# Optimization experiments

Hardware: AMD Instinct MI355X
Metric: run time of the kernel (lower is better)

## Reference

```python
import jax, jax.numpy as jnp
from jax import lax
import numpy as np

ALPHA = 0.5
MAX_ITERS = 40
TOL = 1e-6
BITS = 8


def fake_quant_sym(w, bits=BITS):
    # symmetric per-tensor fake quantisation
    qmax = float(2 ** (bits - 1) - 1)
    scale = jnp.max(jnp.abs(w)) / qmax
    return jnp.round(w / scale) * scale


def fb_solve(Wq, Uq, bq, x, alpha=ALPHA, max_iters=MAX_ITERS, tol=TOL):
    # forward-backward splitting fixed-point solve: z = relu((1-a)z + a(Wz + Ux^T + b))
    n = Wq.shape[0]
    B = x.shape[0]
    Ux = Uq @ x.T + bq[:, None]  # (n, B), constant across iterations

    def cond(carry):
        z, res, it = carry
        return jnp.logical_and(it < max_iters, res >= tol)

    def body(carry):
        z, _, it = carry
        u = (1.0 - alpha) * z + alpha * (Wq @ z + Ux)
        z_next = jax.nn.relu(u)  # relu_prox
        res = jnp.linalg.norm(z_next - z) / (jnp.linalg.norm(z) + 1e-12)
        return z_next, res, it + 1

    z0 = jnp.zeros((n, B), dtype=x.dtype)
    z, _, _ = lax.while_loop(cond, body, (z0, jnp.array(jnp.inf, dtype=x.dtype), 0))
    u_star = (1.0 - alpha) * z + alpha * (Wq @ z + Ux)
    mask = (u_star > 0).astype(x.dtype)  # relu Jacobian mask D*
    return z, mask


def setup_inputs() -> dict:
    key = jax.random.key(0)
    k0, k1, k2, k3, k4 = jax.random.split(key, 5)
    n, d, B, C = 512, 784, 128, 10
    # scale W so ||W||_2 < 1 (monotone operator condition m > 0)
    W = 0.3 * jax.random.normal(k0, (n, n), dtype=jnp.float32) / jnp.sqrt(n)
    U = jax.random.normal(k1, (n, d), dtype=jnp.float32) / jnp.sqrt(d)
    b = 0.01 * jax.random.normal(k2, (n,), dtype=jnp.float32)
    x = jax.random.normal(k3, (B, d), dtype=jnp.float32)
    Wc = jax.random.normal(k4, (C, n), dtype=jnp.float32) / jnp.sqrt(n)
    bc = jnp.zeros((C,), dtype=jnp.float32)
    return {"W": W, "U": U, "b": b, "x": x, "Wc": Wc, "bc": bc}


def reference(W, U, b, x, Wc, bc):
    # post-training fake quantisation of W, U, b (done once at init in torch)
    Wq = fake_quant_sym(W)
    Uq = fake_quant_sym(U)
    bq = fake_quant_sym(b)
    z_star, _ = fb_solve(Wq, Uq, bq, x)  # (n, B)
    logits = z_star.T @ Wc.T + bc  # classifier on z*^T
    return logits
```

## Files before the change

kernel.cpp:

```cpp
#include <hip/hip_runtime.h>
#include <hip/hip_bf16.h>


#define N_DIM 512
#define D_DIM 784
#define B_DIM 128
#define C_DIM 10
#define QMAX 127.0f
#define N_ITERS 40
#define HILO_START 28
#define ZPITCH 528
#define MT 2
#define UPITCH 808

typedef int    i32x4  __attribute__((ext_vector_type(4)));
typedef float  f32x4  __attribute__((ext_vector_type(4)));
typedef __bf16 bf16x8 __attribute__((ext_vector_type(8)));
typedef short  s16x2  __attribute__((ext_vector_type(2)));

__device__ __forceinline__ void pack_hl(const int vq[4], unsigned int& h, unsigned int& l) {
    int pk01, pk23;
#if __has_builtin(__builtin_amdgcn_cvt_pk_i16)
    union { s16x2 v; int i; } u0, u1;
    u0.v = __builtin_amdgcn_cvt_pk_i16(vq[0], vq[1]);
    u1.v = __builtin_amdgcn_cvt_pk_i16(vq[2], vq[3]);
    pk01 = u0.i; pk23 = u1.i;
#else
    asm("v_cvt_pk_i16_i32 %0, %1, %2" : "=v"(pk01) : "v"(vq[0]), "v"(vq[1]));
    asm("v_cvt_pk_i16_i32 %0, %1, %2" : "=v"(pk23) : "v"(vq[2]), "v"(vq[3]));
#endif
    h = __builtin_amdgcn_perm((unsigned int)pk23, (unsigned int)pk01, 0x07050301u);
    l = __builtin_amdgcn_perm((unsigned int)pk23, (unsigned int)pk01, 0x06040200u) ^ 0x80808080u;
}

__global__ __launch_bounds__(256) void prep_kernel(const float* __restrict__ W,
                                                   const float* __restrict__ U,
                                                   const float* __restrict__ b,
                                                   const float* __restrict__ x,
                                                   int* __restrict__ sync,
                                                   signed char* __restrict__ Qp8,
                                                   float* __restrict__ UxT) {
    __shared__ __bf16 xhS[16][UPITCH];
    __shared__ __bf16 xlS[16][UPITCH];
    __shared__ f32x4  sacc[4][64];
    __shared__ float  smax[3];
    const int t = threadIdx.x;
    const int wave = t >> 6, lane = t & 63;

    {
        const int gid = blockIdx.x * 256 + t;
        float mW = 0.0f, mU = 0.0f, mB = 0.0f;
        if (gid < N_DIM * N_DIM / 4) {
            float4 v = ((const float4*)W)[gid];
            mW = fmaxf(fmaxf(fabsf(v.x), fabsf(v.y)), fmaxf(fabsf(v.z), fabsf(v.w)));
        }
        if (gid < N_DIM * D_DIM / 4) {
            float4 v = ((const float4*)U)[gid];
            mU = fmaxf(fmaxf(fabsf(v.x), fabsf(v.y)), fmaxf(fabsf(v.z), fabsf(v.w)));
        }
        if (gid < N_DIM / 4) {
            float4 v = ((const float4*)b)[gid];
            mB = fmaxf(fmaxf(fabsf(v.x), fabsf(v.y)), fmaxf(fabsf(v.z), fabsf(v.w)));
        }
#pragma unroll
        for (int s = 1; s < 64; s <<= 1) {
            mW = fmaxf(mW, __shfl_xor(mW, s));
            mU = fmaxf(mU, __shfl_xor(mU, s));
            mB = fmaxf(mB, __shfl_xor(mB, s));
        }
        float* ls = (float*)sacc;
        if (lane == 0) { ls[wave * 3 + 0] = mW; ls[wave * 3 + 1] = mU; ls[wave * 3 + 2] = mB; }
        __syncthreads();
        if (t == 0) {
            float aW = fmaxf(fmaxf(ls[0], ls[3]), fmaxf(ls[6], ls[9]));
            float aU = fmaxf(fmaxf(ls[1], ls[4]), fmaxf(ls[7], ls[10]));
            float aB = fmaxf(fmaxf(ls[2], ls[5]), fmaxf(ls[8], ls[11]));
            atomicMax(&sync[1], __float_as_int(aW));
            atomicMax(&sync[2], __float_as_int(aU));
            atomicMax(&sync[3], __float_as_int(aB));
            __hip_atomic_fetch_add(&sync[0], 1, __ATOMIC_ACQ_REL, __HIP_MEMORY_SCOPE_AGENT);
            while (__hip_atomic_load(&sync[0], __ATOMIC_ACQUIRE, __HIP_MEMORY_SCOPE_AGENT)
                   < (int)gridDim.x)
                __builtin_amdgcn_s_sleep(2);
            smax[0] = __int_as_float(__hip_atomic_load(&sync[1], __ATOMIC_RELAXED, __HIP_MEMORY_SCOPE_AGENT));
            smax[1] = __int_as_float(__hip_atomic_load(&sync[2], __ATOMIC_RELAXED, __HIP_MEMORY_SCOPE_AGENT));
            smax[2] = __int_as_float(__hip_atomic_load(&sync[3], __ATOMIC_RELAXED, __HIP_MEMORY_SCOPE_AGENT));
        }
        __syncthreads();
    }

    if (blockIdx.x < 256) {
        const float s = smax[0] * (1.0f / QMAX);
        const float inv = 1.0f / s;
        int idx = blockIdx.x * 256 + t;
        float4 w = ((const float4*)W)[idx];
        int k = (idx << 2) & (N_DIM - 1);
        int r = (idx << 2) >> 9;
        char4 c;
        c.x = (signed char)(int)rintf(w.x * inv);
        c.y = (signed char)(int)rintf(w.y * inv);
        c.z = (signed char)(int)rintf(w.z * inv);
        c.w = (signed char)(int)rintf(w.w * inv);
        int kc = k >> 6, q = (k >> 4) & 3, jj = k & 15;
        *(char4*)&Qp8[((kc << 9) + r) * 64 + q * 16 + jj] = c;
    } else {
        const float sU = smax[1] * (1.0f / QMAX);
        const float invU = 1.0f / sU;
        const float sb = smax[2] * (1.0f / QMAX);
        const int bx = blockIdx.x - 256;
        const int i0 = (bx >> 3) * 16;
        const int c0 = (bx & 7) * 16;
        for (int i = t; i < 16 * 196; i += 256) {
            int r = i / 196, kf = i - r * 196;
            float4 v = *(const float4*)&x[(c0 + r) * D_DIM + (kf << 2)];
            union { __bf16 e[4]; ushort4 u; } hh, ll;
            float f0 = v.x, f1 = v.y, f2 = v.z, f3 = v.w;
            __bf16 h0 = (__bf16)f0, h1 = (__bf16)f1, h2 = (__bf16)f2, h3 = (__bf16)f3;
            hh.e[0] = h0; hh.e[1] = h1; hh.e[2] = h2; hh.e[3] = h3;
            ll.e[0] = (__bf16)(f0 - (float)h0);
            ll.e[1] = (__bf16)(f1 - (float)h1);
            ll.e[2] = (__bf16)(f2 - (float)h2);
            ll.e[3] = (__bf16)(f3 - (float)h3);
            *(ushort4*)&xhS[r][kf << 2] = hh.u;
            *(ushort4*)&xlS[r][kf << 2] = ll.u;
        }
        {
            int r = t >> 4, k = D_DIM + (t & 15);
            xhS[r][k] = (__bf16)0.0f; xlS[r][k] = (__bf16)0.0f;
        }
        __syncthreads();
        const int m = lane & 15, quad = lane >> 4;
        f32x4 acc = {};
        for (int kc = wave; kc < 25; kc += 4) {
            const int k0 = (kc << 5) + (quad << 3);
            bf16x8 au = {};
            if (k0 < D_DIM) {
                const float4 u0 = *(const float4*)&U[(i0 + m) * D_DIM + k0];
                const float4 u1 = *(const float4*)&U[(i0 + m) * D_DIM + k0 + 4];
                au[0] = (__bf16)rintf(u0.x * invU); au[1] = (__bf16)rintf(u0.y * invU);
                au[2] = (__bf16)rintf(u0.z * invU); au[3] = (__bf16)rintf(u0.w * invU);
                au[4] = (__bf16)rintf(u1.x * invU); au[5] = (__bf16)rintf(u1.y * invU);
                au[6] = (__bf16)rintf(u1.z * invU); au[7] = (__bf16)rintf(u1.w * invU);
            }
            bf16x8 bh = *(const bf16x8*)&xhS[m][k0];
            bf16x8 bl = *(const bf16x8*)&xlS[m][k0];
            acc = __builtin_amdgcn_mfma_f32_16x16x32_bf16(au, bh, acc, 0, 0, 0);
            acc = __builtin_amdgcn_mfma_f32_16x16x32_bf16(au, bl, acc, 0, 0, 0);
        }
        sacc[wave][lane] = acc;
        __syncthreads();
        if (wave == 0) {
            f32x4 s0 = sacc[0][lane], s1 = sacc[1][lane];
            f32x4 s2 = sacc[2][lane], s3 = sacc[3][lane];
            const int row0 = i0 + (quad << 2);
            f32x4 o;
#pragma unroll
            for (int r = 0; r < 4; ++r)
                o[r] = sU * (s0[r] + s1[r] + s2[r] + s3[r])
                     + rintf(b[row0 + r] / sb) * sb;
            *(f32x4*)&UxT[(c0 + m) * N_DIM + row0] = o;
        }
    }
}

__global__ __launch_bounds__(1024, 1) void solve_kernel(const signed char* __restrict__ Qp8,
                                                        const float* __restrict__ UxT,
                                                        const float* __restrict__ wsf,
                                                        const float* __restrict__ Wc,
                                                        const float* __restrict__ bc,
                                                        float* __restrict__ out) {
    __shared__ signed char zh[2][16][ZPITCH];
    __shared__ signed char zl[2][16][ZPITCH];
    __shared__ float red[16][16][C_DIM];
    const int t = threadIdx.x;
    const int wave = t >> 6;
    const int lane = t & 63;
    const int m = lane & 15;
    const int quad = lane >> 4;
    const int c0 = blockIdx.x * 16;
    const float sW = wsf[1] * (1.0f / QMAX);
    const float c1 = sW * (1.0f / 2048.0f);
    const float hc_hi = c1 * 128.0f;
    const float g_hi = sW * 128.0f;
    const float g_lo = sW * 0.5f;
    const int rowbase = wave * 32;

    i32x4 A[MT][8];
#pragma unroll
    for (int ti = 0; ti < MT; ++ti)
#pragma unroll
        for (int kc = 0; kc < 8; ++kc)
            A[ti][kc] = *(const i32x4*)&Qp8[((kc << 9) + rowbase + ti * 16 + m) * 64 + (quad << 4)];

    const i32x4 onesb = {0x01010101, 0x01010101, 0x01010101, 0x01010101};
    i32x4 rs[MT];
#pragma unroll
    for (int ti = 0; ti < MT; ++ti) {
        i32x4 a = {};
#pragma unroll
        for (int kc = 0; kc < 8; ++kc)
            a = __builtin_amdgcn_mfma_i32_16x16x64_i8(A[ti][kc], onesb, a, 0, 0, 0);
        rs[ti] = a;
    }

    float Z[MT][4];
    float UX2[MT][4];
#pragma unroll
    for (int ti = 0; ti < MT; ++ti) {
        const int row0 = rowbase + ti * 16 + (quad << 2);
        const f32x4 v4 = *(const f32x4*)&UxT[(c0 + m) * N_DIM + row0];
        int vq[4];
#pragma unroll
        for (int r = 0; r < 4; ++r) {
            const float v = v4[r];
            const float uxh = 0.5f * (v + hc_hi * (float)rs[ti][r]);
            UX2[ti][r] = uxh * 2048.0f;
            const float z1 = fmaxf(0.5f * v, 0.0f);
            const float Z1 = z1 * 2048.0f;
            Z[ti][r] = Z1;
            vq[r] = (int)rintf(Z1);
        }
        unsigned int h, l;
        pack_hl(vq, h, l);
        *(unsigned int*)&zh[0][m][row0] = h;
        *(unsigned int*)&zl[0][m][row0] = l;
    }

#pragma unroll
    for (int ti = 0; ti < MT; ++ti)
#pragma unroll
        for (int kc = 0; kc < 8; ++kc)
            asm volatile("" : "+v"(A[ti][kc]));
    __syncthreads();

    int cur = 0;
    for (int it = 1; it < N_ITERS; ++it) {
        const bool lo = (it >= HILO_START);
        const bool wlo = (it >= HILO_START - 1);
        i32x4 acch[MT] = {};
        i32x4 accl[MT] = {};
        if (lo) {
#pragma unroll
            for (int kc = 0; kc < 8; ++kc) {
                i32x4 bh = *(const i32x4*)&zh[cur][m][(kc << 6) + (quad << 4)];
                i32x4 bl = *(const i32x4*)&zl[cur][m][(kc << 6) + (quad << 4)];
#pragma unroll
                for (int ti = 0; ti < MT; ++ti) {
                    acch[ti] = __builtin_amdgcn_mfma_i32_16x16x64_i8(A[ti][kc], bh, acch[ti], 0, 0, 0);
                    accl[ti] = __builtin_amdgcn_mfma_i32_16x16x64_i8(A[ti][kc], bl, accl[ti], 0, 0, 0);
                }
            }
        } else {
#pragma unroll
            for (int kc = 0; kc < 8; ++kc) {
                i32x4 bh = *(const i32x4*)&zh[cur][m][(kc << 6) + (quad << 4)];
#pragma unroll
                for (int ti = 0; ti < MT; ++ti)
                    acch[ti] = __builtin_amdgcn_mfma_i32_16x16x64_i8(A[ti][kc], bh, acch[ti], 0, 0, 0);
            }
        }
        const int nxt = cur ^ 1;
#pragma unroll
        for (int ti = 0; ti < MT; ++ti) {
            const int row0 = rowbase + ti * 16 + (quad << 2);
            int vq[4];
#pragma unroll
            for (int r = 0; r < 4; ++r) {
                float base = fmaf(0.5f, Z[ti][r], UX2[ti][r]);
                float u = lo ? fmaf(g_hi, (float)acch[ti][r], fmaf(g_lo, (float)accl[ti][r], base))
                             : fmaf(g_hi, (float)acch[ti][r], base);
                float Zn = fmaxf(u, 0.0f);
                Z[ti][r] = Zn;
                vq[r] = (int)rintf(Zn);
            }
            unsigned int h, l;
            pack_hl(vq, h, l);
            *(unsigned int*)&zh[nxt][m][row0] = h;
            if (wlo) *(unsigned int*)&zl[nxt][m][row0] = l;
        }
        __syncthreads();
        cur = nxt;
    }

    {
        float p[C_DIM];
#pragma unroll
        for (int cl = 0; cl < C_DIM; ++cl) p[cl] = 0.0f;
#pragma unroll
        for (int ti = 0; ti < MT; ++ti) {
            const int row0 = rowbase + ti * 16 + (quad << 2);
#pragma unroll
            for (int r = 0; r < 4; ++r) {
                float zv = Z[ti][r] * (1.0f / 2048.0f);
#pragma unroll
                for (int cl = 0; cl < C_DIM; ++cl)
                    p[cl] += zv * Wc[cl * N_DIM + row0 + r];
            }
        }
#pragma unroll
        for (int cl = 0; cl < C_DIM; ++cl) {
            p[cl] += __shfl_xor(p[cl], 16);
            p[cl] += __shfl_xor(p[cl], 32);
        }
        if (lane < 16) {
#pragma unroll
            for (int cl = 0; cl < C_DIM; ++cl) red[wave][lane][cl] = p[cl];
        }
        __syncthreads();
        for (int s = 8; s > 0; s >>= 1) {
            if (wave < s && lane < 16) {
#pragma unroll
                for (int cl = 0; cl < C_DIM; ++cl)
                    red[wave][lane][cl] += red[wave + s][lane][cl];
            }
            __syncthreads();
        }
        if (t < 16 * C_DIM) {
            int col = t & 15;
            int cl  = t >> 4;
            out[(c0 + col) * C_DIM + cl] = red[0][col][cl] + bc[cl];
        }
    }
}

extern "C" void kernel_launch(void* const* d_in, const int* in_sizes, int n_in,
                              void* d_out, int out_size, void* d_ws, size_t ws_size,
                              hipStream_t stream) {
    const float* W  = (const float*)d_in[0];
    const float* U  = (const float*)d_in[1];
    const float* b  = (const float*)d_in[2];
    const float* x  = (const float*)d_in[3];
    const float* Wc = (const float*)d_in[4];
    const float* bc = (const float*)d_in[5];
    float* out = (float*)d_out;

    float* ws = (float*)d_ws;
    int* sync = (int*)ws;
    signed char* Qp8 = (signed char*)(ws + 256);
    float* UxT = ws + 256 + (N_DIM * N_DIM / 4);

    hipMemsetAsync(sync, 0, 16, stream);
    prep_kernel<<<512, 256, 0, stream>>>(W, U, b, x, sync, Qp8, UxT);
    solve_kernel<<<8, 1024, 0, stream>>>(Qp8, UxT, ws, Wc, bc, out);
}
```

Baseline: 161.9 us.

## Split grid-wide max barrier into per-tensor counters with partial-max slots

Replaces the single all-block barrier, in which every one of the 512 blocks did atomicMax and waited for the full grid, with dedicated reducer blocks. 64 blocks reduce W, 64 reduce U and 1 reduces b, each writing a partial max into its own slot and bumping a per-tensor counter. Quantize blocks wait only on the counter for the tensor they need, so W-quantize blocks no longer wait on U, and fewer global atomics are issued. The cost is more workspace to clear, a serial read of 64 partials per block, and reliance on the reducer blocks being co-resident with the spinning blocks.

Result: faster. 154.8 us (-4.4%).

```diff
diff --git a/kernel.cpp b/kernel.cpp
--- a/kernel.cpp
+++ b/kernel.cpp
@@ -17,6 +17,14 @@
 typedef float  f32x4  __attribute__((ext_vector_type(4)));
 typedef __bf16 bf16x8 __attribute__((ext_vector_type(8)));
 typedef short  s16x2  __attribute__((ext_vector_type(2)));
+
+#define WS_CNTW 0
+#define WS_CNTU 32
+#define WS_CNTB 64
+#define WS_FIN  72
+#define WS_PW   80
+#define WS_PU   144
+#define WS_PB   208
 
 __device__ __forceinline__ void pack_hl(const int vq[4], unsigned int& h, unsigned int& l) {
     int pk01, pk23;
@@ -46,53 +54,70 @@
     __shared__ float  smax[3];
     const int t = threadIdx.x;
     const int wave = t >> 6, lane = t & 63;
-
-    {
-        const int gid = blockIdx.x * 256 + t;
-        float mW = 0.0f, mU = 0.0f, mB = 0.0f;
-        if (gid < N_DIM * N_DIM / 4) {
-            float4 v = ((const float4*)W)[gid];
-            mW = fmaxf(fmaxf(fabsf(v.x), fabsf(v.y)), fmaxf(fabsf(v.z), fabsf(v.w)));
-        }
-        if (gid < N_DIM * D_DIM / 4) {
-            float4 v = ((const float4*)U)[gid];
-            mU = fmaxf(fmaxf(fabsf(v.x), fabsf(v.y)), fmaxf(fabsf(v.z), fabsf(v.w)));
-        }
-        if (gid < N_DIM / 4) {
-            float4 v = ((const float4*)b)[gid];
-            mB = fmaxf(fmaxf(fabsf(v.x), fabsf(v.y)), fmaxf(fabsf(v.z), fabsf(v.w)));
-        }
-#pragma unroll
-        for (int s = 1; s < 64; s <<= 1) {
-            mW = fmaxf(mW, __shfl_xor(mW, s));
-            mU = fmaxf(mU, __shfl_xor(mU, s));
-            mB = fmaxf(mB, __shfl_xor(mB, s));
-        }
+    const int bid = blockIdx.x;
+
+    int*   cntW = &sync[WS_CNTW];
+    int*   cntU = &sync[WS_CNTU];
+    int*   cntB = &sync[WS_CNTB];
+    float* fin  = (float*)&sync[WS_FIN];
+    float* pW   = (float*)&sync[WS_PW];
+    float* pU   = (float*)&sync[WS_PU];
+    float* pB   = (float*)&sync[WS_PB];
+
+    if (bid < 129) {
+        const float4* src; int n4, rb, nb;
+        if (bid < 64)       { src = (const float4*)W; n4 = N_DIM * N_DIM / 4; rb = bid;      nb = 64; }
+        else if (bid < 128) { src = (const float4*)U; n4 = N_DIM * D_DIM / 4; rb = bid - 64; nb = 64; }
+        else                { src = (const float4*)b; n4 = N_DIM / 4;         rb = 0;        nb = 1;  }
+        float mv = 0.0f;
+        for (int i = rb * 256 + t; i < n4; i += nb * 256) {
+            float4 v = src[i];
+            mv = fmaxf(mv, fmaxf(fmaxf(fabsf(v.x), fabsf(v.y)), fmaxf(fabsf(v.z), fabsf(v.w))));
+        }
+#pragma unroll
+        for (int s = 1; s < 64; s <<= 1) mv = fmaxf(mv, __shfl_xor(mv, s));
         float* ls = (float*)sacc;
-        if (lane == 0) { ls[wave * 3 + 0] = mW; ls[wave * 3 + 1] = mU; ls[wave * 3 + 2] = mB; }
+        if (lane == 0) ls[wave] = mv;
         __syncthreads();
         if (t == 0) {
-            float aW = fmaxf(fmaxf(ls[0], ls[3]), fmaxf(ls[6], ls[9]));
-            float aU = fmaxf(fmaxf(ls[1], ls[4]), fmaxf(ls[7], ls[10]));
-            float aB = fmaxf(fmaxf(ls[2], ls[5]), fmaxf(ls[8], ls[11]));
-            atomicMax(&sync[1], __float_as_int(aW));
-            atomicMax(&sync[2], __float_as_int(aU));
-            atomicMax(&sync[3], __float_as_int(aB));
-            __hip_atomic_fetch_add(&sync[0], 1, __ATOMIC_ACQ_REL, __HIP_MEMORY_SCOPE_AGENT);
-            while (__hip_atomic_load(&sync[0], __ATOMIC_ACQUIRE, __HIP_MEMORY_SCOPE_AGENT)
-                   < (int)gridDim.x)
+            float mm = fmaxf(fmaxf(ls[0], ls[1]), fmaxf(ls[2], ls[3]));
+            float* part = (bid < 64) ? pW : (bid < 128 ? pU : pB);
+            int    rbb  = (bid < 64) ? bid : (bid < 128 ? bid - 64 : 0);
+            int*   cnt  = (bid < 64) ? cntW : (bid < 128 ? cntU : cntB);
+            __hip_atomic_store(&part[rbb], mm, __ATOMIC_RELAXED, __HIP_MEMORY_SCOPE_AGENT);
+            __hip_atomic_fetch_add(cnt, 1, __ATOMIC_RELEASE, __HIP_MEMORY_SCOPE_AGENT);
+        }
+    }
+
+    if (t == 0) {
+        if (bid < 256) {
+            while (__hip_atomic_load(cntW, __ATOMIC_ACQUIRE, __HIP_MEMORY_SCOPE_AGENT) < 64)
                 __builtin_amdgcn_s_sleep(2);
-            smax[0] = __int_as_float(__hip_atomic_load(&sync[1], __ATOMIC_RELAXED, __HIP_MEMORY_SCOPE_AGENT));
-            smax[1] = __int_as_float(__hip_atomic_load(&sync[2], __ATOMIC_RELAXED, __HIP_MEMORY_SCOPE_AGENT));
-            smax[2] = __int_as_float(__hip_atomic_load(&sync[3], __ATOMIC_RELAXED, __HIP_MEMORY_SCOPE_AGENT));
-        }
-        __syncthreads();
-    }
-
-    if (blockIdx.x < 256) {
+            float m = 0.0f;
+#pragma unroll 16
+            for (int i = 0; i < 64; ++i)
+                m = fmaxf(m, __hip_atomic_load(&pW[i], __ATOMIC_RELAXED, __HIP_MEMORY_SCOPE_AGENT));
+            smax[0] = m;
+            if (bid == 0) fin[0] = m;
+        } else {
+            while (__hip_atomic_load(cntU, __ATOMIC_ACQUIRE, __HIP_MEMORY_SCOPE_AGENT) < 64)
+                __builtin_amdgcn_s_sleep(2);
+            while (__hip_atomic_load(cntB, __ATOMIC_ACQUIRE, __HIP_MEMORY_SCOPE_AGENT) < 1)
+                __builtin_amdgcn_s_sleep(2);
+            float mu = 0.0f;
+#pragma unroll 16
+            for (int i = 0; i < 64; ++i)
+                mu = fmaxf(mu, __hip_atomic_load(&pU[i], __ATOMIC_RELAXED, __HIP_MEMORY_SCOPE_AGENT));
+            smax[1] = mu;
+            smax[2] = __hip_atomic_load(&pB[0], __ATOMIC_RELAXED, __HIP_MEMORY_SCOPE_AGENT);
+        }
+    }
+    __syncthreads();
+
+    if (bid < 256) {
         const float s = smax[0] * (1.0f / QMAX);
         const float inv = 1.0f / s;
-        int idx = blockIdx.x * 256 + t;
+        int idx = bid * 256 + t;
         float4 w = ((const float4*)W)[idx];
         int k = (idx << 2) & (N_DIM - 1);
         int r = (idx << 2) >> 9;
@@ -107,7 +132,7 @@
         const float sU = smax[1] * (1.0f / QMAX);
         const float invU = 1.0f / sU;
         const float sb = smax[2] * (1.0f / QMAX);
-        const int bx = blockIdx.x - 256;
+        const int bx = bid - 256;
         const int i0 = (bx >> 3) * 16;
         const int c0 = (bx & 7) * 16;
         for (int i = t; i < 16 * 196; i += 256) {
@@ -178,7 +203,7 @@
     const int m = lane & 15;
     const int quad = lane >> 4;
     const int c0 = blockIdx.x * 16;
-    const float sW = wsf[1] * (1.0f / QMAX);
+    const float sW = wsf[WS_FIN] * (1.0f / QMAX);
     const float c1 = sW * (1.0f / 2048.0f);
     const float hc_hi = c1 * 128.0f;
     const float g_hi = sW * 128.0f;
@@ -339,7 +364,7 @@
     signed char* Qp8 = (signed char*)(ws + 256);
     float* UxT = ws + 256 + (N_DIM * N_DIM / 4);
 
-    hipMemsetAsync(sync, 0, 16, stream);
+    hipMemsetAsync(sync, 0, 320, stream);
     prep_kernel<<<512, 256, 0, stream>>>(W, U, b, x, sync, Qp8, UxT);
     solve_kernel<<<8, 1024, 0, stream>>>(Qp8, UxT, ws, Wc, bc, out);
 }
```

## Split scale reduction into separate kernel, drop grid spin barrier and memset

Applied to the files above, without the earlier changes.

Replaces the in-kernel grid-wide atomic spin barrier and the memset with a separate scales kernel. That kernel writes per-block partial maxima, the quantised bias and a bf16 hi/lo split of x to workspace. The prep kernel then reduces the 64 partials locally, quantises U into shared memory once per 16-row tile, and loops over all 8 column groups, removing redundant U quantisation and x splitting. This adds a kernel launch and extra global round trips for x and the partials, in exchange for removing the serialising barrier.

Result: faster. 142.4 us (-12.0%).

```diff
diff --git a/kernel.cpp b/kernel.cpp
--- a/kernel.cpp
+++ b/kernel.cpp
@@ -11,12 +11,29 @@
 #define HILO_START 28
 #define ZPITCH 528
 #define MT 2
-#define UPITCH 808
+#define XPITCH 800
+#define QUPITCH 808
 
 typedef int    i32x4  __attribute__((ext_vector_type(4)));
 typedef float  f32x4  __attribute__((ext_vector_type(4)));
 typedef __bf16 bf16x8 __attribute__((ext_vector_type(8)));
 typedef short  s16x2  __attribute__((ext_vector_type(2)));
+
+#define WSF_PW  0
+#define WSF_PU  64
+#define WSF_SB  128
+#define WSF_BQ  192
+#define WSF_XH  704
+#define WSF_XL  (WSF_XH + 51200)
+#define WSF_QP8 (WSF_XL + 51200)
+#define WSF_UXT (WSF_QP8 + 65536)
+
+__device__ __forceinline__ float pscale64(const float* __restrict__ p) {
+    float m = 0.0f;
+#pragma unroll 16
+    for (int i = 0; i < 64; ++i) m = fmaxf(m, p[i]);
+    return m * (1.0f / QMAX);
+}
 
 __device__ __forceinline__ void pack_hl(const int vq[4], unsigned int& h, unsigned int& l) {
     int pk01, pk23;
@@ -33,66 +50,91 @@
     l = __builtin_amdgcn_perm((unsigned int)pk23, (unsigned int)pk01, 0x06040200u) ^ 0x80808080u;
 }
 
+__global__ __launch_bounds__(256) void scales_kernel(const float* __restrict__ W,
+                                                     const float* __restrict__ U,
+                                                     const float* __restrict__ b,
+                                                     const float* __restrict__ x,
+                                                     float* __restrict__ ws) {
+    __shared__ float ls[4];
+    __shared__ float sbS;
+    const int t = threadIdx.x, wave = t >> 6, lane = t & 63;
+    const int bid = blockIdx.x;
+    if (bid < 128) {
+        const float4* src; int n4, rb;
+        if (bid < 64) { src = (const float4*)W; n4 = N_DIM * N_DIM / 4; rb = bid; }
+        else          { src = (const float4*)U; n4 = N_DIM * D_DIM / 4; rb = bid - 64; }
+        float mv = 0.0f;
+        for (int i = rb * 256 + t; i < n4; i += 64 * 256) {
+            float4 v = src[i];
+            mv = fmaxf(mv, fmaxf(fmaxf(fabsf(v.x), fabsf(v.y)), fmaxf(fabsf(v.z), fabsf(v.w))));
+        }
+#pragma unroll
+        for (int s = 1; s < 64; s <<= 1) mv = fmaxf(mv, __shfl_xor(mv, s));
+        if (lane == 0) ls[wave] = mv;
+        __syncthreads();
+        if (t == 0) ws[bid] = fmaxf(fmaxf(ls[0], ls[1]), fmaxf(ls[2], ls[3]));
+    } else if (bid == 128) {
+        float4 v = {0.0f, 0.0f, 0.0f, 0.0f};
+        if (t < N_DIM / 4) v = ((const float4*)b)[t];
+        float mv = fmaxf(fmaxf(fabsf(v.x), fabsf(v.y)), fmaxf(fabsf(v.z), fabsf(v.w)));
+#pragma unroll
+        for (int s = 1; s < 64; s <<= 1) mv = fmaxf(mv, __shfl_xor(mv, s));
+        if (lane == 0) ls[wave] = mv;
+        __syncthreads();
+        if (t == 0) {
+            float m = fmaxf(fmaxf(ls[0], ls[1]), fmaxf(ls[2], ls[3]));
+            float sb = m * (1.0f / QMAX);
+            ws[WSF_SB] = sb;
+            sbS = sb;
+        }
+        __syncthreads();
+        if (t < N_DIM / 4) {
+            const float sb = sbS;
+            float4 o;
+            o.x = rintf(v.x / sb) * sb;
+            o.y = rintf(v.y / sb) * sb;
+            o.z = rintf(v.z / sb) * sb;
+            o.w = rintf(v.w / sb) * sb;
+            ((float4*)(ws + WSF_BQ))[t] = o;
+        }
+    } else {
+        __bf16* xh = (__bf16*)(ws + WSF_XH);
+        __bf16* xl = (__bf16*)(ws + WSF_XL);
+        const int xb = bid - 129;
+        for (int i = xb * 256 + t; i < 128 * 196; i += 64 * 256) {
+            int r = i / 196, kf = i - r * 196;
+            float4 v = *(const float4*)&x[r * D_DIM + (kf << 2)];
+            union { __bf16 e[4]; ushort4 u; } hh, ll;
+            __bf16 h0 = (__bf16)v.x, h1 = (__bf16)v.y, h2 = (__bf16)v.z, h3 = (__bf16)v.w;
+            hh.e[0] = h0; hh.e[1] = h1; hh.e[2] = h2; hh.e[3] = h3;
+            ll.e[0] = (__bf16)(v.x - (float)h0);
+            ll.e[1] = (__bf16)(v.y - (float)h1);
+            ll.e[2] = (__bf16)(v.z - (float)h2);
+            ll.e[3] = (__bf16)(v.w - (float)h3);
+            *(ushort4*)&xh[r * XPITCH + (kf << 2)] = hh.u;
+            *(ushort4*)&xl[r * XPITCH + (kf << 2)] = ll.u;
+        }
+        if (xb == 0) {
+            int r = t >> 1, c = D_DIM + (t & 1) * 8;
+            ushort4 z = {0, 0, 0, 0};
+            *(ushort4*)&xh[r * XPITCH + c] = z; *(ushort4*)&xh[r * XPITCH + c + 4] = z;
+            *(ushort4*)&xl[r * XPITCH + c] = z; *(ushort4*)&xl[r * XPITCH + c + 4] = z;
+        }
+    }
+}
+
 __global__ __launch_bounds__(256) void prep_kernel(const float* __restrict__ W,
                                                    const float* __restrict__ U,
-                                                   const float* __restrict__ b,
-                                                   const float* __restrict__ x,
-                                                   int* __restrict__ sync,
-                                                   signed char* __restrict__ Qp8,
-                                                   float* __restrict__ UxT) {
-    __shared__ __bf16 xhS[16][UPITCH];
-    __shared__ __bf16 xlS[16][UPITCH];
-    __shared__ f32x4  sacc[4][64];
-    __shared__ float  smax[3];
+                                                   float* __restrict__ ws,
+                                                   signed char* __restrict__ Qp8) {
+    __shared__ __bf16 quS[16][QUPITCH];
     const int t = threadIdx.x;
     const int wave = t >> 6, lane = t & 63;
-
-    {
-        const int gid = blockIdx.x * 256 + t;
-        float mW = 0.0f, mU = 0.0f, mB = 0.0f;
-        if (gid < N_DIM * N_DIM / 4) {
-            float4 v = ((const float4*)W)[gid];
-            mW = fmaxf(fmaxf(fabsf(v.x), fabsf(v.y)), fmaxf(fabsf(v.z), fabsf(v.w)));
-        }
-        if (gid < N_DIM * D_DIM / 4) {
-            float4 v = ((const float4*)U)[gid];
-            mU = fmaxf(fmaxf(fabsf(v.x), fabsf(v.y)), fmaxf(fabsf(v.z), fabsf(v.w)));
-        }
-        if (gid < N_DIM / 4) {
-            float4 v = ((const float4*)b)[gid];
-            mB = fmaxf(fmaxf(fabsf(v.x), fabsf(v.y)), fmaxf(fabsf(v.z), fabsf(v.w)));
-        }
-#pragma unroll
-        for (int s = 1; s < 64; s <<= 1) {
-            mW = fmaxf(mW, __shfl_xor(mW, s));
-            mU = fmaxf(mU, __shfl_xor(mU, s));
-            mB = fmaxf(mB, __shfl_xor(mB, s));
-        }
-        float* ls = (float*)sacc;
-        if (lane == 0) { ls[wave * 3 + 0] = mW; ls[wave * 3 + 1] = mU; ls[wave * 3 + 2] = mB; }
-        __syncthreads();
-        if (t == 0) {
-            float aW = fmaxf(fmaxf(ls[0], ls[3]), fmaxf(ls[6], ls[9]));
-            float aU = fmaxf(fmaxf(ls[1], ls[4]), fmaxf(ls[7], ls[10]));
-            float aB = fmaxf(fmaxf(ls[2], ls[5]), fmaxf(ls[8], ls[11]));
-            atomicMax(&sync[1], __float_as_int(aW));
-            atomicMax(&sync[2], __float_as_int(aU));
-            atomicMax(&sync[3], __float_as_int(aB));
-            __hip_atomic_fetch_add(&sync[0], 1, __ATOMIC_ACQ_REL, __HIP_MEMORY_SCOPE_AGENT);
-            while (__hip_atomic_load(&sync[0], __ATOMIC_ACQUIRE, __HIP_MEMORY_SCOPE_AGENT)
-                   < (int)gridDim.x)
-                __builtin_amdgcn_s_sleep(2);
-            smax[0] = __int_as_float(__hip_atomic_load(&sync[1], __ATOMIC_RELAXED, __HIP_MEMORY_SCOPE_AGENT));
-            smax[1] = __int_as_float(__hip_atomic_load(&sync[2], __ATOMIC_RELAXED, __HIP_MEMORY_SCOPE_AGENT));
-            smax[2] = __int_as_float(__hip_atomic_load(&sync[3], __ATOMIC_RELAXED, __HIP_MEMORY_SCOPE_AGENT));
-        }
-        __syncthreads();
-    }
-
-    if (blockIdx.x < 256) {
-        const float s = smax[0] * (1.0f / QMAX);
+    const int bid = blockIdx.x;
+    if (bid < 256) {
+        const float s = pscale64(ws + WSF_PW);
         const float inv = 1.0f / s;
-        int idx = blockIdx.x * 256 + t;
+        int idx = bid * 256 + t;
         float4 w = ((const float4*)W)[idx];
         int k = (idx << 2) & (N_DIM - 1);
         int r = (idx << 2) >> 9;
@@ -104,61 +146,44 @@
         int kc = k >> 6, q = (k >> 4) & 3, jj = k & 15;
         *(char4*)&Qp8[((kc << 9) + r) * 64 + q * 16 + jj] = c;
     } else {
-        const float sU = smax[1] * (1.0f / QMAX);
+        const float sU = pscale64(ws + WSF_PU);
         const float invU = 1.0f / sU;
-        const float sb = smax[2] * (1.0f / QMAX);
-        const int bx = blockIdx.x - 256;
-        const int i0 = (bx >> 3) * 16;
-        const int c0 = (bx & 7) * 16;
+        const int i0 = (bid - 256) * 16;
         for (int i = t; i < 16 * 196; i += 256) {
             int r = i / 196, kf = i - r * 196;
-            float4 v = *(const float4*)&x[(c0 + r) * D_DIM + (kf << 2)];
-            union { __bf16 e[4]; ushort4 u; } hh, ll;
-            float f0 = v.x, f1 = v.y, f2 = v.z, f3 = v.w;
-            __bf16 h0 = (__bf16)f0, h1 = (__bf16)f1, h2 = (__bf16)f2, h3 = (__bf16)f3;
-            hh.e[0] = h0; hh.e[1] = h1; hh.e[2] = h2; hh.e[3] = h3;
-            ll.e[0] = (__bf16)(f0 - (float)h0);
-            ll.e[1] = (__bf16)(f1 - (float)h1);
-            ll.e[2] = (__bf16)(f2 - (float)h2);
-            ll.e[3] = (__bf16)(f3 - (float)h3);
-            *(ushort4*)&xhS[r][kf << 2] = hh.u;
-            *(ushort4*)&xlS[r][kf << 2] = ll.u;
-        }
-        {
-            int r = t >> 4, k = D_DIM + (t & 15);
-            xhS[r][k] = (__bf16)0.0f; xlS[r][k] = (__bf16)0.0f;
-        }
+            float4 v = *(const float4*)&U[(i0 + r) * D_DIM + (kf << 2)];
+            union { __bf16 e[4]; ushort4 u; } q;
+            q.e[0] = (__bf16)rintf(v.x * invU);
+            q.e[1] = (__bf16)rintf(v.y * invU);
+            q.e[2] = (__bf16)rintf(v.z * invU);
+            q.e[3] = (__bf16)rintf(v.w * invU);
+            *(ushort4*)&quS[r][kf << 2] = q.u;
+        }
+        { int r = t >> 4, k = D_DIM + (t & 15); quS[r][k] = (__bf16)0.0f; }
         __syncthreads();
         const int m = lane & 15, quad = lane >> 4;
-        f32x4 acc = {};
-        for (int kc = wave; kc < 25; kc += 4) {
-            const int k0 = (kc << 5) + (quad << 3);
-            bf16x8 au = {};
-            if (k0 < D_DIM) {
-                const float4 u0 = *(const float4*)&U[(i0 + m) * D_DIM + k0];
-                const float4 u1 = *(const float4*)&U[(i0 + m) * D_DIM + k0 + 4];
-                au[0] = (__bf16)rintf(u0.x * invU); au[1] = (__bf16)rintf(u0.y * invU);
-                au[2] = (__bf16)rintf(u0.z * invU); au[3] = (__bf16)rintf(u0.w * invU);
-                au[4] = (__bf16)rintf(u1.x * invU); au[5] = (__bf16)rintf(u1.y * invU);
-                au[6] = (__bf16)rintf(u1.z * invU); au[7] = (__bf16)rintf(u1.w * invU);
-            }
-            bf16x8 bh = *(const bf16x8*)&xhS[m][k0];
-            bf16x8 bl = *(const bf16x8*)&xlS[m][k0];
-            acc = __builtin_amdgcn_mfma_f32_16x16x32_bf16(au, bh, acc, 0, 0, 0);
-            acc = __builtin_amdgcn_mfma_f32_16x16x32_bf16(au, bl, acc, 0, 0, 0);
-        }
-        sacc[wave][lane] = acc;
-        __syncthreads();
-        if (wave == 0) {
-            f32x4 s0 = sacc[0][lane], s1 = sacc[1][lane];
-            f32x4 s2 = sacc[2][lane], s3 = sacc[3][lane];
-            const int row0 = i0 + (quad << 2);
+        const __bf16* xh = (const __bf16*)(ws + WSF_XH);
+        const __bf16* xl = (const __bf16*)(ws + WSF_XL);
+        const float* bq = ws + WSF_BQ;
+        float* UxT = ws + WSF_UXT;
+        const int row0 = i0 + (quad << 2);
+        const f32x4 bqv = *(const f32x4*)&bq[row0];
+        for (int cg = wave; cg < 8; cg += 4) {
+            const __bf16* xhr = &xh[(cg * 16 + m) * XPITCH];
+            const __bf16* xlr = &xl[(cg * 16 + m) * XPITCH];
+            f32x4 acc = {};
+#pragma unroll 5
+            for (int kc = 0; kc < 25; ++kc) {
+                bf16x8 au = *(const bf16x8*)&quS[m][kc * 32 + (quad << 3)];
+                bf16x8 bh = *(const bf16x8*)&xhr[kc * 32 + (quad << 3)];
+                bf16x8 bl = *(const bf16x8*)&xlr[kc * 32 + (quad << 3)];
+                acc = __builtin_amdgcn_mfma_f32_16x16x32_bf16(au, bh, acc, 0, 0, 0);
+                acc = __builtin_amdgcn_mfma_f32_16x16x32_bf16(au, bl, acc, 0, 0, 0);
+            }
             f32x4 o;
 #pragma unroll
-            for (int r = 0; r < 4; ++r)
-                o[r] = sU * (s0[r] + s1[r] + s2[r] + s3[r])
-                     + rintf(b[row0 + r] / sb) * sb;
-            *(f32x4*)&UxT[(c0 + m) * N_DIM + row0] = o;
+            for (int r = 0; r < 4; ++r) o[r] = sU * acc[r] + bqv[r];
+            *(f32x4*)&UxT[(cg * 16 + m) * N_DIM + row0] = o;
         }
     }
 }
@@ -178,7 +203,7 @@
     const int m = lane & 15;
     const int quad = lane >> 4;
     const int c0 = blockIdx.x * 16;
-    const float sW = wsf[1] * (1.0f / QMAX);
+    const float sW = pscale64(wsf + WSF_PW);
     const float c1 = sW * (1.0f / 2048.0f);
     const float hc_hi = c1 * 128.0f;
     const float g_hi = sW * 128.0f;
@@ -335,11 +360,10 @@
     float* out = (float*)d_out;
 
     float* ws = (float*)d_ws;
-    int* sync = (int*)ws;
-    signed char* Qp8 = (signed char*)(ws + 256);
-    float* UxT = ws + 256 + (N_DIM * N_DIM / 4);
-
-    hipMemsetAsync(sync, 0, 16, stream);
-    prep_kernel<<<512, 256, 0, stream>>>(W, U, b, x, sync, Qp8, UxT);
+    signed char* Qp8 = (signed char*)(ws + WSF_QP8);
+    float* UxT = ws + WSF_UXT;
+
+    scales_kernel<<<193, 256, 0, stream>>>(W, U, b, x, ws);
+    prep_kernel<<<288, 256, 0, stream>>>(W, U, ws, Qp8);
     solve_kernel<<<8, 1024, 0, stream>>>(Qp8, UxT, ws, Wc, bc, out);
 }
```
